# Optimization experiments

Measured on AMD Instinct MI355X. Metric: run time of the kernel, lower is better.

The kernel has to match this reference:

```python
import jax, jax.numpy as jnp
import numpy as np
from jax import lax

VOCAB = 50000
EMB = 256
HID = 512          # bidirectional output dim
H = HID // 2       # per-direction hidden size
B = 32
T = 1024
K = 14             # 12 entities + START + STOP
START = K - 2
STOP = K - 1


def setup_inputs() -> dict:
    key = jax.random.key(0)
    ks = jax.random.split(key, 16)
    rn = lambda k, shape, s=0.05: (jax.random.normal(k, shape, jnp.float32) * s)
    crf = jax.random.normal(ks[14], (K, K), jnp.float32)
    # forbid transitions into START and out of STOP (as in torch init)
    crf = crf.at[:, START].set(-1000.0).at[STOP, :].set(-1000.0)
    return {
        "sentences": jax.random.randint(ks[0], (B, T), 0, VOCAB),
        "emb": rn(ks[1], (VOCAB, EMB), 1.0),
        "Wih_f": rn(ks[2], (4 * H, EMB)), "Whh_f": rn(ks[3], (4 * H, H)),
        "bih_f": rn(ks[4], (4 * H,)), "bhh_f": rn(ks[5], (4 * H,)),
        "Wih_b": rn(ks[6], (4 * H, EMB)), "Whh_b": rn(ks[7], (4 * H, H)),
        "bih_b": rn(ks[8], (4 * H,)), "bhh_b": rn(ks[9], (4 * H,)),
        "h0": rn(ks[10], (2, B, H), 1.0),  # [dir, B, H] like torch init_hidden randn
        "c0": rn(ks[11], (2, B, H), 1.0),
        "W_out": rn(ks[12], (K, HID)), "b_out": rn(ks[13], (K,)),
        "crf": crf,
    }


def _lstm_dir(x, h0, c0, Wih, Whh, bih, bhh, reverse):
    # x: [B, T, E] -> hs: [B, T, H]; PyTorch gate order i, f, g, o
    def step(carry, xt):
        h, c = carry
        g = xt @ Wih.T + bih + h @ Whh.T + bhh  # [B, 4H]
        i, f, gg, o = jnp.split(g, 4, axis=-1)
        c = jax.nn.sigmoid(f) * c + jax.nn.sigmoid(i) * jnp.tanh(gg)
        h = jax.nn.sigmoid(o) * jnp.tanh(c)
        return (h, c), h
    _, hs = lax.scan(step, (h0, c0), jnp.swapaxes(x, 0, 1), reverse=reverse)
    return jnp.swapaxes(hs, 0, 1)


def _viterbi(logits, crf):
    # logits: [T, K]; max-plus recurrence over time
    def step(prev, lt):
        v = prev[:, None] + crf          # [K, K]: from-tag x to-tag
        return lt + jnp.max(v, axis=0), jnp.argmax(v, axis=0)
    last, bps = lax.scan(step, logits[0], logits[1:])  # bps: [T-1, K]
    score = jnp.max(last)
    last_tag = jnp.argmax(last)
    def back(tag, bp):
        p = bp[tag]
        return p, p
    _, rest = lax.scan(back, last_tag, bps, reverse=True)  # path[0..T-2]
    path = jnp.concatenate([rest, last_tag[None]])
    return score, path


def reference(sentences, emb, Wih_f, Whh_f, bih_f, bhh_f,
              Wih_b, Whh_b, bih_b, bhh_b, h0, c0, W_out, b_out, crf):
    x = emb[sentences]  # [B, T, E]
    hf = _lstm_dir(x, h0[0], c0[0], Wih_f, Whh_f, bih_f, bhh_f, False)
    hb = _lstm_dir(x, h0[1], c0[1], Wih_b, Whh_b, bih_b, bhh_b, True)
    hs = jnp.concatenate([hf, hb], axis=-1)        # [B, T, HID]
    logits = hs @ W_out.T + b_out                  # [B, T, K]
    scores, paths = jax.vmap(lambda l: _viterbi(l, crf))(logits)
    return scores, paths
```

## Files before the change

kernel.cpp:

```cpp
#include <hip/hip_runtime.h>
#include <hip/hip_bf16.h>
#include <cstdint>

#define B_ 32
#define T_ 1024
#define E_ 256
#define H_ 256
#define G_ 1024
#define NTAG 14
#define LOG2E 1.4426950408889634f

typedef __bf16 bf8_t __attribute__((ext_vector_type(8)));
typedef float f4_t __attribute__((ext_vector_type(4)));
typedef int i4_t __attribute__((ext_vector_type(4)));
typedef unsigned short u16x4 __attribute__((ext_vector_type(4)));

__device__ __forceinline__ unsigned short f2bf(float f) {
    unsigned u = __builtin_bit_cast(unsigned, f);
    u = u + 0x7FFFu + ((u >> 16) & 1u);
    return (unsigned short)(u >> 16);
}
__device__ __forceinline__ float bf2f(unsigned short s) {
    unsigned u = ((unsigned)s) << 16;
    return __builtin_bit_cast(float, u);
}
__device__ __forceinline__ float fexp2(float x) { return __builtin_amdgcn_exp2f(x); }
__device__ __forceinline__ float frcp(float x) { return __builtin_amdgcn_rcpf(x); }
__device__ __forceinline__ float sigf(float x) {
    return frcp(1.0f + fexp2(-LOG2E * x));
}
__device__ __forceinline__ float tanh2_(float x) {
    return 1.0f - 2.0f * frcp(fexp2((2.0f * LOG2E) * x) + 1.0f);
}
__device__ __forceinline__ f4_t mfma16(bf8_t a, bf8_t b, f4_t c) {
    return __builtin_amdgcn_mfma_f32_16x16x32_bf16(a, b, c, 0, 0, 0);
}

__global__ __launch_bounds__(256) void setup_kernel(
        const int* sent, const float* emb,
        const float* whh_f, const float* whh_b,
        const float* wih_f, const float* wih_b,
        const float* bih_f, const float* bhh_f,
        const float* bih_b, const float* bhh_b,
        const float* wout,
        unsigned short* xbf, signed char* qw, float* sw,
        unsigned short* wih_bf, float* biasc, unsigned short* wout_bf) {
    int bid = blockIdx.x, thr = threadIdx.x;
    if (bid < 8192) {
        int tid = bid * 256 + thr;
        int bt = tid >> 6;
        int e0 = (tid & 63) << 2;
        int tok = sent[bt];
        float4 v = *reinterpret_cast<const float4*>(emb + (size_t)tok * E_ + e0);
        u16x4 o;
        o[0] = f2bf(v.x); o[1] = f2bf(v.y); o[2] = f2bf(v.z); o[3] = f2bf(v.w);
        *reinterpret_cast<u16x4*>(xbf + (size_t)bt * E_ + e0) = o;
        return;
    }
    if (bid < 8704) {
        int row = (bid - 8192) * 4 + (thr >> 6);
        int l = thr & 63;
        int d = row >> 10, rr = row & 1023;
        const float* src = (d ? whh_b : whh_f) + (size_t)rr * 256;
        float4 v = *reinterpret_cast<const float4*>(src + 4 * l);
        float am = fmaxf(fmaxf(fabsf(v.x), fabsf(v.y)), fmaxf(fabsf(v.z), fabsf(v.w)));
#pragma unroll
        for (int off = 1; off < 64; off <<= 1)
            am = fmaxf(am, __shfl_xor(am, off));
        am = fmaxf(am, 1e-20f);
        float inv = 127.f / am;
        int q0 = (int)__builtin_rintf(v.x * inv), q1 = (int)__builtin_rintf(v.y * inv);
        int q2 = (int)__builtin_rintf(v.z * inv), q3 = (int)__builtin_rintf(v.w * inv);
        unsigned u = (q0 & 255) | ((q1 & 255) << 8) | ((q2 & 255) << 16) | ((q3 & 255) << 24);
        *reinterpret_cast<unsigned*>(qw + (size_t)row * 256 + 4 * l) = u;
        if (l == 0) sw[row] = am / 127.f;
        return;
    }
    int tid = (bid - 8704) * 256 + thr;
    if (tid < 524288) {
        int d = tid >> 18, off = tid & 262143;
        wih_bf[tid] = f2bf((d ? wih_b : wih_f)[off]);
        return;
    }
    int t2 = tid - 524288;
    if (t2 < 8192) {
        int n = t2 >> 9, k = t2 & 511;
        wout_bf[t2] = (n < NTAG) ? f2bf(wout[n * 512 + k]) : (unsigned short)0;
        return;
    }
    int t3 = t2 - 8192;
    if (t3 < 2048) {
        int d = t3 >> 10, g = t3 & 1023;
        biasc[t3] = d ? (bih_b[g] + bhh_b[g]) : (bih_f[g] + bhh_f[g]);
    }
}

__global__ __launch_bounds__(256, 1) void xproj_kernel(const unsigned short* xbf,
        const unsigned short* wih_bf, const float* biasc, unsigned short* xg4) {
    int tt = blockIdx.x;
    int y = blockIdx.y;
    int ns = y & 3, bh = (y >> 2) & 1, d = y >> 3;
    int w = threadIdx.x >> 6, l = threadIdx.x & 63;
    int l15 = l & 15, lgp = l >> 4;
    __shared__ unsigned short sh[256][16];

    int nbase = ns * 256 + w * 64;
    const unsigned short* wd = wih_bf + (size_t)d * 262144;
    bf8_t breg[4][8];
    float bias[4];
#pragma unroll
    for (int p = 0; p < 4; ++p) {
        int n = nbase + 16 * p + l15;
        bias[p] = biasc[d * G_ + n];
        const unsigned short* brow = wd + (size_t)n * E_ + 8 * lgp;
#pragma unroll
        for (int ks = 0; ks < 8; ++ks)
            breg[p][ks] = *reinterpret_cast<const bf8_t*>(brow + 32 * ks);
    }
#pragma unroll
    for (int p = 0; p < 4; ++p)
#pragma unroll
        for (int ks = 0; ks < 8; ++ks)
            asm volatile("" : "+v"(breg[p][ks]));

    const unsigned short* arow =
        xbf + ((size_t)(16 * bh + l15) * 1024 + tt * 16) * E_ + 8 * lgp;

    for (int it = 0; it < 16; ++it) {
        int t = tt * 16 + it;
        bf8_t a[8];
#pragma unroll
        for (int ks = 0; ks < 8; ++ks)
            a[ks] = *reinterpret_cast<const bf8_t*>(arow + 32 * ks);
        arow += 256;

        f4_t acc[4];
#pragma unroll
        for (int p = 0; p < 4; ++p) { acc[p][0] = 0.f; acc[p][1] = 0.f; acc[p][2] = 0.f; acc[p][3] = 0.f; }
#pragma unroll
        for (int p = 0; p < 4; ++p)
#pragma unroll
            for (int ks = 0; ks < 8; ++ks)
                acc[p] = mfma16(a[ks], breg[p][ks], acc[p]);

#pragma unroll
        for (int p = 0; p < 4; ++p)
#pragma unroll
            for (int r = 0; r < 4; ++r)
                sh[w * 64 + 16 * p + l15][4 * lgp + r] = f2bf(acc[p][r] + bias[p]);
        __syncthreads();
        int q = threadIdx.x;
#pragma unroll
        for (int p = 0; p < 8; ++p) {
            int b2g = 8 * bh + p;
            size_t base = ((size_t)(d * 16 + b2g) * 1024 + t) * 2048 + ns * 256 + q;
            xg4[base]        = sh[q][2 * p];
            xg4[base + 1024] = sh[q][2 * p + 1];
        }
        __syncthreads();
    }
}

__global__ __launch_bounds__(512, 2) void lstm_kernel(const unsigned short* xg4,
        const signed char* qw, const float* sw, const float* h0, const float* c0,
        unsigned short* hs) {
    int bid = blockIdx.x;
    int b2 = bid & 15, d = bid >> 4;
    int tid = threadIdx.x;
    int w = tid >> 6, l = tid & 63, l15 = l & 15, lgp = l >> 4;

    __shared__ __attribute__((aligned(16))) signed char h8[2][2][320];
    __shared__ float red_sh[8];

    const signed char* qwd = qw + (size_t)d * 262144;

    i4_t wreg[4][2][4];
#pragma unroll
    for (int gt = 0; gt < 4; ++gt)
#pragma unroll
        for (int jt = 0; jt < 2; ++jt) {
            int n = 256 * gt + 32 * w + 16 * jt + l15;
#pragma unroll
            for (int ks = 0; ks < 4; ++ks)
                wreg[gt][jt][ks] = *reinterpret_cast<const i4_t*>(
                    qwd + (size_t)n * 256 + 64 * ks + 16 * lgp);
        }
#pragma unroll
    for (int gt = 0; gt < 4; ++gt)
#pragma unroll
        for (int jt = 0; jt < 2; ++jt)
#pragma unroll
            for (int ks = 0; ks < 4; ++ks)
                asm volatile("" : "+v"(wreg[gt][jt][ks]));

    int jt_c = lgp & 1, m_c = lgp >> 1;
    int j = 32 * w + 16 * jt_c + l15;

    float swv[4];
#pragma unroll
    for (int gt = 0; gt < 4; ++gt)
        swv[gt] = sw[d * 1024 + 256 * gt + j];
    float c = c0[((size_t)d * 32 + b2 * 2 + m_c) * 256 + j];

    int im = tid >> 8, ij = tid & 255;
    float v0 = h0[((size_t)d * 32 + b2 * 2 + im) * 256 + ij];
    float am = fabsf(v0);
#pragma unroll
    for (int off = 1; off < 64; off <<= 1)
        am = fmaxf(am, __shfl_xor(am, off));
    if (l == 0) red_sh[w] = am;
    __syncthreads();
    float bmax = red_sh[0];
#pragma unroll
    for (int q = 1; q < 8; ++q) bmax = fmaxf(bmax, red_sh[q]);
    bmax = fmaxf(bmax, 1e-20f);
    float s0 = bmax / 127.f;
    h8[1][im][ij] = (signed char)(int)__builtin_rintf(v0 * (127.f / bmax));

    float dq[4];
#pragma unroll
    for (int gt = 0; gt < 4; ++gt) dq[gt] = swv[gt] * s0;

    int t0 = d ? 1023 : 0;
    int xinc = d ? -2048 : 2048;
    int hinc = d ? -512 : 512;
    const unsigned short* xq = xg4 + ((size_t)(d * 16 + b2) * 1024 + t0) * 2048
                               + m_c * 1024 + j;
    unsigned short* hsp = hs + ((size_t)(b2 * 2 + m_c) * 1024 + t0) * 512 + d * 256 + j;

    unsigned short xc[4], xn[4];
#pragma unroll
    for (int gt = 0; gt < 4; ++gt) xc[gt] = xq[256 * gt];

    i4_t z4 = (i4_t){0, 0, 0, 0};
    asm volatile("" : "+v"(z4));

    __syncthreads();

    for (int s = 0; s < 1024; ++s) {
        int rp = (s + 1) & 1, wp = s & 1;

        if (s < 1023) {
            xq += xinc;
#pragma unroll
            for (int gt = 0; gt < 4; ++gt) xn[gt] = xq[256 * gt];
        }

        i4_t a[4];
#pragma unroll
        for (int ks = 0; ks < 4; ++ks)
            a[ks] = *reinterpret_cast<const i4_t*>(&h8[rp][l15 & 1][64 * ks + 16 * lgp]);

        i4_t acc[4][2];
#pragma unroll
        for (int gt = 0; gt < 4; ++gt)
#pragma unroll
            for (int jt = 0; jt < 2; ++jt) {
                acc[gt][jt] = __builtin_amdgcn_mfma_i32_16x16x64_i8(
                    a[0], wreg[gt][jt][0], z4, 0, 0, 0);
#pragma unroll
                for (int ks = 1; ks < 4; ++ks)
                    acc[gt][jt] = __builtin_amdgcn_mfma_i32_16x16x64_i8(
                        a[ks], wreg[gt][jt][ks], acc[gt][jt], 0, 0, 0);
            }

        int gi[4];
#pragma unroll
        for (int gt = 0; gt < 4; ++gt) {
            int e0 = jt_c ? acc[gt][1][0] : acc[gt][0][0];
            int e1 = jt_c ? acc[gt][1][1] : acc[gt][0][1];
            gi[gt] = m_c ? e1 : e0;
        }

        float pi = dq[0] * (float)gi[0] + bf2f(xc[0]);
        float pf = dq[1] * (float)gi[1] + bf2f(xc[1]);
        float pg = dq[2] * (float)gi[2] + bf2f(xc[2]);
        float po = dq[3] * (float)gi[3] + bf2f(xc[3]);
        float iv = sigf(pi), fv = sigf(pf), ov = sigf(po);
        float gv = tanh2_(pg);
        float cn = fv * c + iv * gv;
        c = cn;
        float hv = ov * tanh2_(cn);
        *hsp = f2bf(hv);
        hsp += hinc;
        h8[wp][m_c][j] = (signed char)(int)__builtin_rintf(hv * 127.f);

        if (s == 0) {
#pragma unroll
            for (int gt = 0; gt < 4; ++gt) dq[gt] = swv[gt] * (1.f / 127.f);
        }
#pragma unroll
        for (int gt = 0; gt < 4; ++gt) xc[gt] = xn[gt];

        asm volatile("s_waitcnt lgkmcnt(0)" ::: "memory");
        __builtin_amdgcn_sched_barrier(0);
        __builtin_amdgcn_s_barrier();
    }
}

__global__ __launch_bounds__(256) void logits_kernel(const unsigned short* hs,
        const unsigned short* wout_bf, const float* b_out, float* logits) {
    int w = threadIdx.x >> 6, l = threadIdx.x & 63, l15 = l & 15, lgp = l >> 4;
    int mt = blockIdx.x * 4 + w;
    const unsigned short* arow = hs + (size_t)(16 * mt + l15) * 512 + 8 * lgp;
    const unsigned short* brow = wout_bf + (size_t)l15 * 512 + 8 * lgp;
    f4_t acc; acc[0] = 0.f; acc[1] = 0.f; acc[2] = 0.f; acc[3] = 0.f;
#pragma unroll
    for (int ks = 0; ks < 16; ++ks) {
        bf8_t a = *reinterpret_cast<const bf8_t*>(arow + 32 * ks);
        bf8_t b = *reinterpret_cast<const bf8_t*>(brow + 32 * ks);
        acc = mfma16(a, b, acc);
    }
    float bo = (l15 < NTAG) ? b_out[l15] : 0.0f;
#pragma unroll
    for (int r = 0; r < 4; ++r) {
        int bt = 16 * mt + 4 * lgp + r;
        logits[(size_t)bt * 16 + l15] = acc[r] + bo;
    }
}

__global__ __launch_bounds__(64) void viterbi_kernel(const float* logits, const float* crf,
                                                     float* out) {
    int b = blockIdx.x, j = threadIdx.x;
    __shared__ unsigned char bp[1024][16];
    __shared__ unsigned char pth[1024];
    float crfj[NTAG];
#pragma unroll
    for (int i = 0; i < NTAG; ++i)
        crfj[i] = (j < NTAG) ? crf[i * NTAG + j] : 0.0f;
    const float* lgt = logits + (size_t)b * 1024 * 16;
    float v = (j < NTAG) ? lgt[j] : -3.0e38f;
    float lt_nxt = (j < NTAG) ? lgt[16 + j] : 0.0f;
    for (int t = 1; t < 1024; ++t) {
        float lt = lt_nxt;
        if (t < 1023) lt_nxt = (j < NTAG) ? lgt[(t + 1) * 16 + j] : 0.0f;
        float sv[NTAG];
#pragma unroll
        for (int i = 0; i < NTAG; ++i)
            sv[i] = __shfl(v, i) + crfj[i];
        float av[7]; int ai[7];
#pragma unroll
        for (int i = 0; i < 7; ++i) {
            bool rgt = sv[2 * i + 1] > sv[2 * i];
            av[i] = rgt ? sv[2 * i + 1] : sv[2 * i];
            ai[i] = rgt ? 2 * i + 1 : 2 * i;
        }
        float bv[4]; int bi[4];
#pragma unroll
        for (int i = 0; i < 3; ++i) {
            bool rgt = av[2 * i + 1] > av[2 * i];
            bv[i] = rgt ? av[2 * i + 1] : av[2 * i];
            bi[i] = rgt ? ai[2 * i + 1] : ai[2 * i];
        }
        bv[3] = av[6]; bi[3] = ai[6];
        float cv0 = (bv[1] > bv[0]) ? bv[1] : bv[0];
        int   ci0 = (bv[1] > bv[0]) ? bi[1] : bi[0];
        float cv1 = (bv[3] > bv[2]) ? bv[3] : bv[2];
        int   ci1 = (bv[3] > bv[2]) ? bi[3] : bi[2];
        float best = (cv1 > cv0) ? cv1 : cv0;
        int   arg  = (cv1 > cv0) ? ci1 : ci0;
        v = (j < NTAG) ? (lt + best) : -3.0e38f;
        if (j < 16) bp[t][j] = (unsigned char)arg;
    }
    float best = -3.0e38f; int tag = 0;
#pragma unroll
    for (int jj = 0; jj < NTAG; ++jj) {
        float s = __shfl(v, jj);
        if (s > best) { best = s; tag = jj; }
    }
    __syncthreads();
    if (j == 0) {
        out[b] = best;
        int tg = tag;
        pth[1023] = (unsigned char)tg;
        for (int t = 1023; t >= 1; --t) {
            tg = bp[t][tg];
            pth[t - 1] = (unsigned char)tg;
        }
    }
    __syncthreads();
    float* pout = out + 32 + (size_t)b * 1024;
    for (int t = j; t < 1024; t += 64)
        pout[t] = (float)pth[t];
}

extern "C" void kernel_launch(void* const* d_in, const int* in_sizes, int n_in,
                              void* d_out, int out_size, void* d_ws, size_t ws_size,
                              hipStream_t stream) {
    const int* sent = (const int*)d_in[0];
    const float* emb = (const float*)d_in[1];
    const float* wih_f = (const float*)d_in[2];
    const float* whh_f = (const float*)d_in[3];
    const float* bih_f = (const float*)d_in[4];
    const float* bhh_f = (const float*)d_in[5];
    const float* wih_b = (const float*)d_in[6];
    const float* whh_b = (const float*)d_in[7];
    const float* bih_b = (const float*)d_in[8];
    const float* bhh_b = (const float*)d_in[9];
    const float* h0 = (const float*)d_in[10];
    const float* c0 = (const float*)d_in[11];
    const float* wout = (const float*)d_in[12];
    const float* b_out = (const float*)d_in[13];
    const float* crf = (const float*)d_in[14];

    char* ws = (char*)d_ws;
    signed char* qw       = (signed char*)(ws + 0);
    float* sw             = (float*)(ws + 524288);
    unsigned short* wih_bf = (unsigned short*)(ws + 1048576);
    float* biasc          = (float*)(ws + 2097152);
    unsigned short* wout_bf = (unsigned short*)(ws + 2105344);
    unsigned short* xbf   = (unsigned short*)(ws + 2121728);
    unsigned short* xg4   = (unsigned short*)(ws + 18898944);
    unsigned short* hs    = (unsigned short*)(ws + 153116672);
    float* logits         = (float*)(ws + 186671104);
    float* out = (float*)d_out;

    hipLaunchKernelGGL(setup_kernel, dim3(10792), dim3(256), 0, stream,
                       sent, emb, whh_f, whh_b, wih_f, wih_b,
                       bih_f, bhh_f, bih_b, bhh_b, wout,
                       xbf, qw, sw, wih_bf, biasc, wout_bf);
    hipLaunchKernelGGL(xproj_kernel, dim3(64, 16), dim3(256), 0, stream,
                       xbf, wih_bf, biasc, xg4);
    hipLaunchKernelGGL(lstm_kernel, dim3(32), dim3(512), 0, stream,
                       xg4, qw, sw, h0, c0, hs);
    hipLaunchKernelGGL(logits_kernel, dim3(512), dim3(256), 0, stream,
                       hs, wout_bf, b_out, logits);
    hipLaunchKernelGGL(viterbi_kernel, dim3(32), dim3(64), 0, stream, logits, crf, out);
}
```

Measured before the change: 1.326 ms.

## Fuse logits projection into Viterbi kernel and simplify argmax

Removes the separate logits kernel. Each Viterbi block now computes its sequence's 1024x16 logits with MFMA into shared memory, then one wavefront runs the max-plus recurrence reading from LDS instead of global memory. The argmax tree is replaced by an fmax reduction plus an equality bitmask and ctz, which keeps first-index tie-breaking. This saves a launch and a global round trip for the logits, but the projection now runs on only 32 blocks instead of 512, so that phase has less parallelism.

Result: faster. 1.168 ms (-11.9%).

```diff
diff --git a/kernel.cpp b/kernel.cpp
--- a/kernel.cpp
+++ b/kernel.cpp
@@ -298,89 +298,81 @@
     }
 }
 
-__global__ __launch_bounds__(256) void logits_kernel(const unsigned short* hs,
-        const unsigned short* wout_bf, const float* b_out, float* logits) {
-    int w = threadIdx.x >> 6, l = threadIdx.x & 63, l15 = l & 15, lgp = l >> 4;
-    int mt = blockIdx.x * 4 + w;
-    const unsigned short* arow = hs + (size_t)(16 * mt + l15) * 512 + 8 * lgp;
-    const unsigned short* brow = wout_bf + (size_t)l15 * 512 + 8 * lgp;
-    f4_t acc; acc[0] = 0.f; acc[1] = 0.f; acc[2] = 0.f; acc[3] = 0.f;
-#pragma unroll
-    for (int ks = 0; ks < 16; ++ks) {
-        bf8_t a = *reinterpret_cast<const bf8_t*>(arow + 32 * ks);
-        bf8_t b = *reinterpret_cast<const bf8_t*>(brow + 32 * ks);
-        acc = mfma16(a, b, acc);
-    }
-    float bo = (l15 < NTAG) ? b_out[l15] : 0.0f;
-#pragma unroll
-    for (int r = 0; r < 4; ++r) {
-        int bt = 16 * mt + 4 * lgp + r;
-        logits[(size_t)bt * 16 + l15] = acc[r] + bo;
-    }
-}
-
-__global__ __launch_bounds__(64) void viterbi_kernel(const float* logits, const float* crf,
-                                                     float* out) {
-    int b = blockIdx.x, j = threadIdx.x;
+__global__ __launch_bounds__(256) void viterbi_kernel(const unsigned short* hs,
+        const unsigned short* wout_bf, const float* b_out, const float* crf,
+        float* out) {
+    int b = blockIdx.x;
+    int tid = threadIdx.x;
+    int ww = tid >> 6, l = tid & 63, l15 = l & 15, lgp = l >> 4;
+
+    __shared__ float lg[1024][16];
     __shared__ unsigned char bp[1024][16];
     __shared__ unsigned char pth[1024];
-    float crfj[NTAG];
-#pragma unroll
-    for (int i = 0; i < NTAG; ++i)
-        crfj[i] = (j < NTAG) ? crf[i * NTAG + j] : 0.0f;
-    const float* lgt = logits + (size_t)b * 1024 * 16;
-    float v = (j < NTAG) ? lgt[j] : -3.0e38f;
-    float lt_nxt = (j < NTAG) ? lgt[16 + j] : 0.0f;
-    for (int t = 1; t < 1024; ++t) {
-        float lt = lt_nxt;
-        if (t < 1023) lt_nxt = (j < NTAG) ? lgt[(t + 1) * 16 + j] : 0.0f;
-        float sv[NTAG];
+
+    float bo = (l15 < NTAG) ? b_out[l15] : 0.0f;
+    const unsigned short* brow = wout_bf + (size_t)l15 * 512 + 8 * lgp;
+    for (int k = 0; k < 16; ++k) {
+        int mt = ww + 4 * k;
+        const unsigned short* arow = hs + ((size_t)b * 1024 + mt * 16 + l15) * 512 + 8 * lgp;
+        f4_t acc; acc[0] = 0.f; acc[1] = 0.f; acc[2] = 0.f; acc[3] = 0.f;
+#pragma unroll
+        for (int ks = 0; ks < 16; ++ks) {
+            bf8_t a = *reinterpret_cast<const bf8_t*>(arow + 32 * ks);
+            bf8_t bb = *reinterpret_cast<const bf8_t*>(brow + 32 * ks);
+            acc = mfma16(a, bb, acc);
+        }
+#pragma unroll
+        for (int r = 0; r < 4; ++r)
+            lg[mt * 16 + 4 * lgp + r][l15] = acc[r] + bo;
+    }
+    __syncthreads();
+
+    if (ww == 0) {
+        int j = l;
+        float crfj[NTAG];
 #pragma unroll
         for (int i = 0; i < NTAG; ++i)
-            sv[i] = __shfl(v, i) + crfj[i];
-        float av[7]; int ai[7];
-#pragma unroll
-        for (int i = 0; i < 7; ++i) {
-            bool rgt = sv[2 * i + 1] > sv[2 * i];
-            av[i] = rgt ? sv[2 * i + 1] : sv[2 * i];
-            ai[i] = rgt ? 2 * i + 1 : 2 * i;
-        }
-        float bv[4]; int bi[4];
-#pragma unroll
-        for (int i = 0; i < 3; ++i) {
-            bool rgt = av[2 * i + 1] > av[2 * i];
-            bv[i] = rgt ? av[2 * i + 1] : av[2 * i];
-            bi[i] = rgt ? ai[2 * i + 1] : ai[2 * i];
-        }
-        bv[3] = av[6]; bi[3] = ai[6];
-        float cv0 = (bv[1] > bv[0]) ? bv[1] : bv[0];
-        int   ci0 = (bv[1] > bv[0]) ? bi[1] : bi[0];
-        float cv1 = (bv[3] > bv[2]) ? bv[3] : bv[2];
-        int   ci1 = (bv[3] > bv[2]) ? bi[3] : bi[2];
-        float best = (cv1 > cv0) ? cv1 : cv0;
-        int   arg  = (cv1 > cv0) ? ci1 : ci0;
-        v = (j < NTAG) ? (lt + best) : -3.0e38f;
-        if (j < 16) bp[t][j] = (unsigned char)arg;
-    }
-    float best = -3.0e38f; int tag = 0;
-#pragma unroll
-    for (int jj = 0; jj < NTAG; ++jj) {
-        float s = __shfl(v, jj);
-        if (s > best) { best = s; tag = jj; }
-    }
-    __syncthreads();
-    if (j == 0) {
-        out[b] = best;
-        int tg = tag;
-        pth[1023] = (unsigned char)tg;
-        for (int t = 1023; t >= 1; --t) {
-            tg = bp[t][tg];
-            pth[t - 1] = (unsigned char)tg;
+            crfj[i] = (j < NTAG) ? crf[i * NTAG + j] : 0.0f;
+        float v = (j < NTAG) ? lg[0][j] : -3.0e38f;
+        for (int t = 1; t < 1024; ++t) {
+            float sv[NTAG];
+#pragma unroll
+            for (int i = 0; i < NTAG; ++i)
+                sv[i] = __shfl(v, i) + crfj[i];
+            float m0 = fmaxf(fmaxf(sv[0], sv[1]), sv[2]);
+            float m1 = fmaxf(fmaxf(sv[3], sv[4]), sv[5]);
+            float m2 = fmaxf(fmaxf(sv[6], sv[7]), sv[8]);
+            float m3 = fmaxf(fmaxf(sv[9], sv[10]), sv[11]);
+            float m4 = fmaxf(sv[12], sv[13]);
+            float best = fmaxf(fmaxf(fmaxf(m0, m1), fmaxf(m2, m3)), m4);
+            unsigned msk = 0;
+#pragma unroll
+            for (int i = 0; i < NTAG; ++i)
+                msk |= (sv[i] == best) ? (1u << i) : 0u;
+            int arg = __builtin_ctz(msk);
+            float lt = (j < NTAG) ? lg[t][j] : 0.0f;
+            v = (j < NTAG) ? (lt + best) : -3.0e38f;
+            if (j < 16) bp[t][j] = (unsigned char)arg;
+        }
+        float best = -3.0e38f; int tag = 0;
+#pragma unroll
+        for (int jj = 0; jj < NTAG; ++jj) {
+            float s = __shfl(v, jj);
+            if (s > best) { best = s; tag = jj; }
+        }
+        if (j == 0) {
+            out[b] = best;
+            int tg = tag;
+            pth[1023] = (unsigned char)tg;
+            for (int t = 1023; t >= 1; --t) {
+                tg = bp[t][tg];
+                pth[t - 1] = (unsigned char)tg;
+            }
         }
     }
     __syncthreads();
     float* pout = out + 32 + (size_t)b * 1024;
-    for (int t = j; t < 1024; t += 64)
+    for (int t = tid; t < 1024; t += 256)
         pout[t] = (float)pth[t];
 }
 
@@ -412,7 +404,6 @@
     unsigned short* xbf   = (unsigned short*)(ws + 2121728);
     unsigned short* xg4   = (unsigned short*)(ws + 18898944);
     unsigned short* hs    = (unsigned short*)(ws + 153116672);
-    float* logits         = (float*)(ws + 186671104);
     float* out = (float*)d_out;
 
     hipLaunchKernelGGL(setup_kernel, dim3(10792), dim3(256), 0, stream,
@@ -423,7 +414,6 @@
                        xbf, wih_bf, biasc, xg4);
     hipLaunchKernelGGL(lstm_kernel, dim3(32), dim3(512), 0, stream,
                        xg4, qw, sw, h0, c0, hs);
-    hipLaunchKernelGGL(logits_kernel, dim3(512), dim3(256), 0, stream,
-                       hs, wout_bf, b_out, logits);
-    hipLaunchKernelGGL(viterbi_kernel, dim3(32), dim3(64), 0, stream, logits, crf, out);
-}
+    hipLaunchKernelGGL(viterbi_kernel, dim3(32), dim3(256), 0, stream,
+                       hs, wout_bf, b_out, crf, out);
+}
```
